# Kernel optimization log

Measured on AMD Instinct MI355X. Metric: run time of the kernel, lower is better.

Reference implementation:

```python
import jax, jax.numpy as jnp
from jax import lax
import numpy as np

N_INPUTS = 2048
UNITS = 2048
L = 8
FANIN = 4096
TOTAL = N_INPUTS + L * UNITS  # 18432, size of flattened outputs vector


def setup_inputs() -> dict:
    key = jax.random.key(0)
    k1, k2, k3, k4 = jax.random.split(key, 4)
    x = jax.random.normal(k1, (N_INPUTS,), dtype=jnp.float32)
    node_inds = jax.random.randint(k2, (L, FANIN), 0, TOTAL, dtype=jnp.int32)
    # 0.02 scale keeps tanh out of deep saturation (matches small evolved weights)
    Ws = jax.random.normal(k3, (L, FANIN, UNITS), dtype=jnp.float32) * 0.02
    bs = jax.random.normal(k4, (L, UNITS), dtype=jnp.float32) * 0.02
    return {"x": x, "node_inds": node_inds, "Ws": Ws, "bs": bs}


def reference(x, node_inds, Ws, bs):
    # Flattened shared state vector, zero-initialized like the tf.Variable.
    outputs = jnp.zeros((TOTAL,), dtype=x.dtype)
    start = 0  # static python offset: out_update_inds are contiguous ranges
    for i in range(L):
        # scatter_nd_update of x into contiguous slice == dynamic_update_slice
        outputs = lax.dynamic_update_slice(outputs, x, (start,))
        start += x.shape[0]
        # gather node-specific indices then tiny Dense + tanh
        gathered = jnp.take(outputs, node_inds[i])          # [FANIN]
        x = jnp.tanh(gathered @ Ws[i] + bs[i])              # [UNITS]
    return x
```

## Files before the change

kernel.cpp:

```cpp
#include <hip/hip_runtime.h>
#include <cmath>

#define N_INPUTS 2048
#define UNITS    2048
#define L_LAYERS 8
#define FANIN    4096
#define TOTAL    18432

#define NTHREADS 256
#define RK       16
#define KC       (FANIN / RK)
#define JTILE    1024
#define P_BLOCKS (2 * KC)

__device__ __forceinline__ float col_reduce(const float* __restrict__ P, int col)
{
    int lane = threadIdx.x & 63;
    float s = 0.f;
    #pragma unroll
    for (int m = 0; m < KC / 64; ++m)
        s += P[(size_t)(lane + m * 64) * UNITS + col];
    #pragma unroll
    for (int off = 32; off; off >>= 1)
        s += __shfl_down(s, off, 64);
    return __shfl(s, 0, 64);
}

__global__ __launch_bounds__(NTHREADS) void layer_kernel(
    int layer,
    const float* __restrict__ x,
    const int*   __restrict__ node_inds,
    const float* __restrict__ Ws,
    const float* __restrict__ bs,
    float*       __restrict__ outputs,
    const float* __restrict__ Pprev,
    float*       __restrict__ Pcur)
{
    const int b    = blockIdx.x;
    const int t    = threadIdx.x;
    const int wv   = t >> 6;
    const int lane = t & 63;
    const int jhalf = b & 1;
    const int kc    = b >> 1;

    __shared__ float gsh[RK];

    {
        int col = b * 4 + wv;
        if (layer == 0) {
            if (lane == 0) outputs[col] = x[col];
        } else {
            float s = col_reduce(Pprev, col);
            float y = tanhf(s + bs[(layer - 1) * UNITS + col]);
            if (lane == 0) outputs[(size_t)layer * UNITS + col] = y;
        }
    }

    #pragma unroll
    for (int j = 0; j < 4; ++j) {
        int q   = wv * 4 + j;
        int idx = node_inds[layer * FANIN + kc * RK + q];
        float g;
        if (layer == 0) {
            g = (idx < N_INPUTS) ? x[idx] : 0.f;
        } else if (idx < layer * UNITS) {
            g = outputs[idx];
        } else if (idx < (layer + 1) * UNITS) {
            int col = idx - layer * UNITS;
            float s = col_reduce(Pprev, col);
            g = tanhf(s + bs[(layer - 1) * UNITS + col]);
        } else {
            g = 0.f;
        }
        if (lane == 0) gsh[q] = g;
    }
    __syncthreads();

    const int jbase = jhalf * JTILE + t * 4;
    const float4* W4 = (const float4*)(
        Ws + ((size_t)layer * FANIN + (size_t)kc * RK) * UNITS + jbase);

    float4 a; a.x = 0.f; a.y = 0.f; a.z = 0.f; a.w = 0.f;
    #pragma unroll
    for (int k = 0; k < RK; ++k) {
        float  g = gsh[k];
        float4 w = W4[(size_t)k * (UNITS / 4)];
        a.x += g * w.x; a.y += g * w.y; a.z += g * w.z; a.w += g * w.w;
    }
    *(float4*)(Pcur + (size_t)kc * UNITS + jbase) = a;
}

__global__ __launch_bounds__(NTHREADS) void tail_kernel(
    const float* __restrict__ Pprev,
    const float* __restrict__ bs,
    float*       __restrict__ out)
{
    int wv   = threadIdx.x >> 6;
    int lane = threadIdx.x & 63;
    int col  = blockIdx.x * 4 + wv;
    float s = col_reduce(Pprev, col);
    float y = tanhf(s + bs[(L_LAYERS - 1) * UNITS + col]);
    if (lane == 0) out[col] = y;
}

extern "C" void kernel_launch(void* const* d_in, const int* in_sizes, int n_in,
                              void* d_out, int out_size, void* d_ws, size_t ws_size,
                              hipStream_t stream) {
    const float* x         = (const float*)d_in[0];
    const int*   node_inds = (const int*)  d_in[1];
    const float* Ws        = (const float*)d_in[2];
    const float* bs        = (const float*)d_in[3];
    float*       out       = (float*)d_out;
    float*       ws        = (float*)d_ws;

    float* outputs = ws;
    float* P0      = ws + TOTAL;
    float* P1      = P0 + (size_t)KC * UNITS;

    float* pbuf[2] = { P0, P1 };

    for (int i = 0; i < L_LAYERS; ++i) {
        layer_kernel<<<P_BLOCKS, NTHREADS, 0, stream>>>(
            i, x, node_inds, Ws, bs, outputs,
            pbuf[(i + 1) & 1],
            pbuf[i & 1]);
    }
    tail_kernel<<<UNITS / 4, NTHREADS, 0, stream>>>(
        pbuf[(L_LAYERS - 1) & 1], bs, out);
}
```

Baseline: 417.8 us.

## Fuse all layers into one cooperative persistent kernel with register weight prefetch

Replaces the per-layer kernel launches and the tail kernel with a single cooperative kernel that uses grid-wide syncs between layers. Each block keeps its weight tile in registers and prefetches the next layer's weights and indices before the grid sync, so weight loads can overlap the synchronization. This removes launch gaps, but adds grid-sync cost and register pressure, and keeps the original multi-launch path as a fallback if the cooperative launch fails.

```diff
diff --git a/kernel.cpp b/kernel.cpp
--- a/kernel.cpp
+++ b/kernel.cpp
@@ -1,5 +1,8 @@
 #include <hip/hip_runtime.h>
+#include <hip/hip_cooperative_groups.h>
 #include <cmath>
+
+namespace cg = cooperative_groups;
 
 #define N_INPUTS 2048
 #define UNITS    2048
@@ -24,6 +27,109 @@
     for (int off = 32; off; off >>= 1)
         s += __shfl_down(s, off, 64);
     return __shfl(s, 0, 64);
+}
+
+__global__ __launch_bounds__(NTHREADS, 2) void fused_kernel(
+    const float* __restrict__ x,
+    const int*   __restrict__ node_inds,
+    const float* __restrict__ Ws,
+    const float* __restrict__ bs,
+    float*       __restrict__ outputs,
+    float*       __restrict__ out,
+    float*       __restrict__ P0,
+    float*       __restrict__ P1)
+{
+    cg::grid_group grid = cg::this_grid();
+
+    const int b     = blockIdx.x;
+    const int t     = threadIdx.x;
+    const int wv    = t >> 6;
+    const int lane  = t & 63;
+    const int jhalf = b & 1;
+    const int kc    = b >> 1;
+    const int jbase = jhalf * JTILE + t * 4;
+
+    __shared__ float gsh[RK];
+
+    float* pb[2] = { P0, P1 };
+
+    float4 w[RK];
+    {
+        const float4* W4 = (const float4*)(
+            Ws + ((size_t)kc * RK) * UNITS + jbase);
+        #pragma unroll
+        for (int k = 0; k < RK; ++k)
+            w[k] = W4[(size_t)k * (UNITS / 4)];
+    }
+    int4 nidx = *(const int4*)(node_inds + kc * RK + wv * 4);
+
+    for (int lay = 0; lay < L_LAYERS; ++lay) {
+        const float* Pprev = pb[(lay + 1) & 1];
+        float*       Pcur  = pb[lay & 1];
+
+        if (lay > 0) grid.sync();
+
+        {
+            int col = b * 4 + wv;
+            if (lay == 0) {
+                if (lane == 0) outputs[col] = x[col];
+            } else {
+                float s = col_reduce(Pprev, col);
+                float y = tanhf(s + bs[(lay - 1) * UNITS + col]);
+                if (lane == 0) outputs[(size_t)lay * UNITS + col] = y;
+            }
+        }
+
+        {
+            int idxs[4] = { nidx.x, nidx.y, nidx.z, nidx.w };
+            #pragma unroll
+            for (int j = 0; j < 4; ++j) {
+                int q   = wv * 4 + j;
+                int idx = idxs[j];
+                float g;
+                if (lay == 0) {
+                    g = (idx < N_INPUTS) ? x[idx] : 0.f;
+                } else if (idx < lay * UNITS) {
+                    g = outputs[idx];
+                } else if (idx < (lay + 1) * UNITS) {
+                    int col = idx - lay * UNITS;
+                    float s = col_reduce(Pprev, col);
+                    g = tanhf(s + bs[(lay - 1) * UNITS + col]);
+                } else {
+                    g = 0.f;
+                }
+                if (lane == 0) gsh[q] = g;
+            }
+        }
+        __syncthreads();
+
+        float4 a; a.x = 0.f; a.y = 0.f; a.z = 0.f; a.w = 0.f;
+        #pragma unroll
+        for (int k = 0; k < RK; ++k) {
+            float g = gsh[k];
+            a.x += g * w[k].x; a.y += g * w[k].y;
+            a.z += g * w[k].z; a.w += g * w[k].w;
+        }
+        *(float4*)(Pcur + (size_t)kc * UNITS + jbase) = a;
+
+        if (lay + 1 < L_LAYERS) {
+            const float4* W4n = (const float4*)(
+                Ws + ((size_t)(lay + 1) * FANIN + (size_t)kc * RK) * UNITS + jbase);
+            #pragma unroll
+            for (int k = 0; k < RK; ++k)
+                w[k] = W4n[(size_t)k * (UNITS / 4)];
+            nidx = *(const int4*)(
+                node_inds + (lay + 1) * FANIN + kc * RK + wv * 4);
+        }
+    }
+
+    grid.sync();
+    {
+        int col = b * 4 + wv;
+        float s = col_reduce(pb[(L_LAYERS - 1) & 1], col);
+        float y = tanhf(s + bs[(L_LAYERS - 1) * UNITS + col]);
+        if (lane == 0) out[col] = y;
+    }
 }
 
 __global__ __launch_bounds__(NTHREADS) void layer_kernel(
@@ -84,8 +190,8 @@
     #pragma unroll
     for (int k = 0; k < RK; ++k) {
         float  g = gsh[k];
-        float4 w = W4[(size_t)k * (UNITS / 4)];
-        a.x += g * w.x; a.y += g * w.y; a.z += g * w.z; a.w += g * w.w;
+        float4 wv4 = W4[(size_t)k * (UNITS / 4)];
+        a.x += g * wv4.x; a.y += g * wv4.y; a.z += g * wv4.z; a.w += g * wv4.w;
     }
     *(float4*)(Pcur + (size_t)kc * UNITS + jbase) = a;
 }
@@ -117,14 +223,21 @@
     float* P0      = ws + TOTAL;
     float* P1      = P0 + (size_t)KC * UNITS;
 
-    float* pbuf[2] = { P0, P1 };
-
-    for (int i = 0; i < L_LAYERS; ++i) {
-        layer_kernel<<<P_BLOCKS, NTHREADS, 0, stream>>>(
-            i, x, node_inds, Ws, bs, outputs,
-            pbuf[(i + 1) & 1],
-            pbuf[i & 1]);
-    }
-    tail_kernel<<<UNITS / 4, NTHREADS, 0, stream>>>(
-        pbuf[(L_LAYERS - 1) & 1], bs, out);
-}
+    void* args[8] = { (void*)&x, (void*)&node_inds, (void*)&Ws, (void*)&bs,
+                      (void*)&outputs, (void*)&out, (void*)&P0, (void*)&P1 };
+
+    hipError_t e = hipLaunchCooperativeKernel(
+        (const void*)fused_kernel, dim3(P_BLOCKS), dim3(NTHREADS),
+        args, 0, stream);
+
+    if (e != hipSuccess) {
+        float* pbuf[2] = { P0, P1 };
+        for (int i = 0; i < L_LAYERS; ++i) {
+            layer_kernel<<<P_BLOCKS, NTHREADS, 0, stream>>>(
+                i, x, node_inds, Ws, bs, outputs,
+                pbuf[(i + 1) & 1], pbuf[i & 1]);
+        }
+        tail_kernel<<<UNITS / 4, NTHREADS, 0, stream>>>(
+            pbuf[(L_LAYERS - 1) & 1], bs, out);
+    }
+}
```

After: 868.3 us. 108% more time.

## Prefetch weights before gather, transpose partial-sum layout, split columns four ways

Applied to the files above, without the earlier changes.

Each block now issues all of its weight loads into registers before the gather and column-reduce work, so the HBM stream overlaps that latency-bound phase. The partial-sum buffer is transposed to column-major [UNITS][KC], which makes col_reduce reads contiguous per wave but makes the partial-sum stores strided. Blocks split the output columns into four parts, doubling the block count, and launch bounds request higher occupancy. Risks are the scattered 4-byte stores and more register pressure from holding the weights.

```diff
diff --git a/kernel.cpp b/kernel.cpp
--- a/kernel.cpp
+++ b/kernel.cpp
@@ -10,8 +10,9 @@
 #define NTHREADS 256
 #define RK       16
 #define KC       (FANIN / RK)
-#define JTILE    1024
-#define P_BLOCKS (2 * KC)
+#define JPARTS   4
+#define JTILE    (UNITS / JPARTS)
+#define P_BLOCKS (KC * JPARTS)
 
 __device__ __forceinline__ float col_reduce(const float* __restrict__ P, int col)
 {
@@ -19,14 +20,14 @@
     float s = 0.f;
     #pragma unroll
     for (int m = 0; m < KC / 64; ++m)
-        s += P[(size_t)(lane + m * 64) * UNITS + col];
+        s += P[(size_t)col * KC + lane + m * 64];
     #pragma unroll
     for (int off = 32; off; off >>= 1)
         s += __shfl_down(s, off, 64);
     return __shfl(s, 0, 64);
 }
 
-__global__ __launch_bounds__(NTHREADS) void layer_kernel(
+__global__ __launch_bounds__(NTHREADS, 4) void layer_kernel(
     int layer,
     const float* __restrict__ x,
     const int*   __restrict__ node_inds,
@@ -40,13 +41,23 @@
     const int t    = threadIdx.x;
     const int wv   = t >> 6;
     const int lane = t & 63;
-    const int jhalf = b & 1;
-    const int kc    = b >> 1;
+    const int kc   = b >> 2;
+    const int jp   = b & 3;
+    const int jbase = jp * JTILE + t * 2;
 
     __shared__ float gsh[RK];
 
-    {
-        int col = b * 4 + wv;
+    float2 w[RK];
+    const float2* W2 = (const float2*)(
+        Ws + ((size_t)layer * FANIN + (size_t)kc * RK) * UNITS + jbase);
+    #pragma unroll
+    for (int k = 0; k < RK; ++k)
+        w[k] = W2[(size_t)k * (UNITS / 2)];
+
+    int4 nidx = *(const int4*)(node_inds + layer * FANIN + kc * RK + wv * 4);
+
+    if (wv < 2) {
+        int col = b * 2 + wv;
         if (layer == 0) {
             if (lane == 0) outputs[col] = x[col];
         } else {
@@ -56,38 +67,38 @@
         }
     }
 
-    #pragma unroll
-    for (int j = 0; j < 4; ++j) {
-        int q   = wv * 4 + j;
-        int idx = node_inds[layer * FANIN + kc * RK + q];
-        float g;
-        if (layer == 0) {
-            g = (idx < N_INPUTS) ? x[idx] : 0.f;
-        } else if (idx < layer * UNITS) {
-            g = outputs[idx];
-        } else if (idx < (layer + 1) * UNITS) {
-            int col = idx - layer * UNITS;
-            float s = col_reduce(Pprev, col);
-            g = tanhf(s + bs[(layer - 1) * UNITS + col]);
-        } else {
-            g = 0.f;
+    {
+        int idxs[4] = { nidx.x, nidx.y, nidx.z, nidx.w };
+        #pragma unroll
+        for (int j = 0; j < 4; ++j) {
+            int q   = wv * 4 + j;
+            int idx = idxs[j];
+            float g;
+            if (layer == 0) {
+                g = (idx < N_INPUTS) ? x[idx] : 0.f;
+            } else if (idx < layer * UNITS) {
+                g = outputs[idx];
+            } else if (idx < (layer + 1) * UNITS) {
+                int col = idx - layer * UNITS;
+                float s = col_reduce(Pprev, col);
+                g = tanhf(s + bs[(layer - 1) * UNITS + col]);
+            } else {
+                g = 0.f;
+            }
+            if (lane == 0) gsh[q] = g;
         }
-        if (lane == 0) gsh[q] = g;
     }
     __syncthreads();
 
-    const int jbase = jhalf * JTILE + t * 4;
-    const float4* W4 = (const float4*)(
-        Ws + ((size_t)layer * FANIN + (size_t)kc * RK) * UNITS + jbase);
-
-    float4 a; a.x = 0.f; a.y = 0.f; a.z = 0.f; a.w = 0.f;
+    float ax = 0.f, ay = 0.f;
     #pragma unroll
     for (int k = 0; k < RK; ++k) {
-        float  g = gsh[k];
-        float4 w = W4[(size_t)k * (UNITS / 4)];
-        a.x += g * w.x; a.y += g * w.y; a.z += g * w.z; a.w += g * w.w;
+        float g = gsh[k];
+        ax += g * w[k].x;
+        ay += g * w[k].y;
     }
-    *(float4*)(Pcur + (size_t)kc * UNITS + jbase) = a;
+    Pcur[(size_t)jbase       * KC + kc] = ax;
+    Pcur[(size_t)(jbase + 1) * KC + kc] = ay;
 }
 
 __global__ __launch_bounds__(NTHREADS) void tail_kernel(
```

Result: faster. 399.6 us (-4.3%).

## Replace partial-sum matrix and column reductions with atomic accumulation

Applied to the files above, without the earlier changes.

Each block now reduces its 64-row K-chunk in shared memory and atomically adds into a 2048-wide accumulator. This replaces writing a 256x2048 partial matrix and re-reducing columns for every gathered index. Three rotating accumulator buffers let each layer zero the next buffer while reading the previous one, so gathers become single loads plus tanh. Weight loads are issued into registers before the gather and the sync, to hide latency. The cost is float atomic contention and run-to-run rounding differences from unordered accumulation.

```diff
diff --git a/kernel.cpp b/kernel.cpp
--- a/kernel.cpp
+++ b/kernel.cpp
@@ -8,99 +8,106 @@
 #define TOTAL    18432
 
 #define NTHREADS 256
-#define RK       16
+#define RK       64
 #define KC       (FANIN / RK)
-#define JTILE    1024
-#define P_BLOCKS (2 * KC)
+#define JTILE    128
+#define JPARTS   (UNITS / JTILE)
+#define P_BLOCKS (KC * JPARTS)
 
-__device__ __forceinline__ float col_reduce(const float* __restrict__ P, int col)
-{
-    int lane = threadIdx.x & 63;
-    float s = 0.f;
-    #pragma unroll
-    for (int m = 0; m < KC / 64; ++m)
-        s += P[(size_t)(lane + m * 64) * UNITS + col];
-    #pragma unroll
-    for (int off = 32; off; off >>= 1)
-        s += __shfl_down(s, off, 64);
-    return __shfl(s, 0, 64);
-}
-
-__global__ __launch_bounds__(NTHREADS) void layer_kernel(
+__global__ __launch_bounds__(NTHREADS, 4) void layer_kernel(
     int layer,
     const float* __restrict__ x,
     const int*   __restrict__ node_inds,
     const float* __restrict__ Ws,
     const float* __restrict__ bs,
     float*       __restrict__ outputs,
-    const float* __restrict__ Pprev,
-    float*       __restrict__ Pcur)
+    const float* __restrict__ accPrev,
+    float*       __restrict__ accCur,
+    float*       __restrict__ accNext)
 {
-    const int b    = blockIdx.x;
-    const int t    = threadIdx.x;
-    const int wv   = t >> 6;
-    const int lane = t & 63;
-    const int jhalf = b & 1;
-    const int kc    = b >> 1;
+    const int b  = blockIdx.x;
+    const int t  = threadIdx.x;
+    const int kc = b >> 4;
+    const int jp = b & 15;
+    const int jbase = jp * JTILE;
+    const int g  = t >> 5;
+    const int c0 = (t & 31) * 4;
 
-    __shared__ float gsh[RK];
+    __shared__ float  gsh[RK];
+    __shared__ float4 red[8][32];
 
-    {
-        int col = b * 4 + wv;
+    int idx = 0;
+    if (t < RK) idx = node_inds[layer * FANIN + kc * RK + t];
+
+    const float* Wp = Ws
+        + ((size_t)layer * FANIN + (size_t)kc * RK + (size_t)g * 8) * UNITS
+        + jbase + c0;
+    float4 w[8];
+    #pragma unroll
+    for (int r = 0; r < 8; ++r)
+        w[r] = *(const float4*)(Wp + (size_t)r * UNITS);
+
+    if (t < RK) {
+        float v;
         if (layer == 0) {
-            if (lane == 0) outputs[col] = x[col];
+            v = (idx < N_INPUTS) ? x[idx] : 0.f;
+        } else if (idx < layer * UNITS) {
+            v = outputs[idx];
+        } else if (idx < (layer + 1) * UNITS) {
+            int col = idx - layer * UNITS;
+            v = tanhf(accPrev[col] + bs[(layer - 1) * UNITS + col]);
         } else {
-            float s = col_reduce(Pprev, col);
-            float y = tanhf(s + bs[(layer - 1) * UNITS + col]);
-            if (lane == 0) outputs[(size_t)layer * UNITS + col] = y;
+            v = 0.f;
+        }
+        gsh[t] = v;
+    }
+
+    if (kc == 0 && t < JTILE) {
+        int col = jbase + t;
+        if (layer == 0) {
+            outputs[col] = x[col];
+        } else {
+            float y = tanhf(accPrev[col] + bs[(layer - 1) * UNITS + col]);
+            outputs[(size_t)layer * UNITS + col] = y;
         }
     }
 
-    #pragma unroll
-    for (int j = 0; j < 4; ++j) {
-        int q   = wv * 4 + j;
-        int idx = node_inds[layer * FANIN + kc * RK + q];
-        float g;
-        if (layer == 0) {
-            g = (idx < N_INPUTS) ? x[idx] : 0.f;
-        } else if (idx < layer * UNITS) {
-            g = outputs[idx];
-        } else if (idx < (layer + 1) * UNITS) {
-            int col = idx - layer * UNITS;
-            float s = col_reduce(Pprev, col);
-            g = tanhf(s + bs[(layer - 1) * UNITS + col]);
-        } else {
-            g = 0.f;
-        }
-        if (lane == 0) gsh[q] = g;
-    }
+    if (t < 2) accNext[b * 2 + t] = 0.f;
+
     __syncthreads();
-
-    const int jbase = jhalf * JTILE + t * 4;
-    const float4* W4 = (const float4*)(
-        Ws + ((size_t)layer * FANIN + (size_t)kc * RK) * UNITS + jbase);
 
     float4 a; a.x = 0.f; a.y = 0.f; a.z = 0.f; a.w = 0.f;
     #pragma unroll
-    for (int k = 0; k < RK; ++k) {
-        float  g = gsh[k];
-        float4 w = W4[(size_t)k * (UNITS / 4)];
-        a.x += g * w.x; a.y += g * w.y; a.z += g * w.z; a.w += g * w.w;
+    for (int r = 0; r < 8; ++r) {
+        float gg = gsh[g * 8 + r];
+        a.x += gg * w[r].x; a.y += gg * w[r].y;
+        a.z += gg * w[r].z; a.w += gg * w[r].w;
     }
-    *(float4*)(Pcur + (size_t)kc * UNITS + jbase) = a;
+    red[g][t & 31] = a;
+    __syncthreads();
+
+    if (t < 32) {
+        float4 s = red[0][t];
+        #pragma unroll
+        for (int q = 1; q < 8; ++q) {
+            float4 r4 = red[q][t];
+            s.x += r4.x; s.y += r4.y; s.z += r4.z; s.w += r4.w;
+        }
+        int col = jbase + t * 4;
+        atomicAdd(accCur + col + 0, s.x);
+        atomicAdd(accCur + col + 1, s.y);
+        atomicAdd(accCur + col + 2, s.z);
+        atomicAdd(accCur + col + 3, s.w);
+    }
 }
 
 __global__ __launch_bounds__(NTHREADS) void tail_kernel(
-    const float* __restrict__ Pprev,
+    const float* __restrict__ acc,
     const float* __restrict__ bs,
     float*       __restrict__ out)
 {
-    int wv   = threadIdx.x >> 6;
-    int lane = threadIdx.x & 63;
-    int col  = blockIdx.x * 4 + wv;
-    float s = col_reduce(Pprev, col);
-    float y = tanhf(s + bs[(L_LAYERS - 1) * UNITS + col]);
-    if (lane == 0) out[col] = y;
+    int i = blockIdx.x * NTHREADS + threadIdx.x;
+    out[i] = tanhf(acc[i] + bs[(L_LAYERS - 1) * UNITS + i]);
 }
 
 extern "C" void kernel_launch(void* const* d_in, const int* in_sizes, int n_in,
@@ -114,17 +121,20 @@
     float*       ws        = (float*)d_ws;
 
     float* outputs = ws;
-    float* P0      = ws + TOTAL;
-    float* P1      = P0 + (size_t)KC * UNITS;
+    float* A0      = ws + TOTAL;
+    float* A1      = A0 + UNITS;
+    float* A2      = A1 + UNITS;
+    float* bufs[3] = { A0, A1, A2 };
 
-    float* pbuf[2] = { P0, P1 };
+    hipMemsetAsync(A0, 0, UNITS * sizeof(float), stream);
 
     for (int i = 0; i < L_LAYERS; ++i) {
         layer_kernel<<<P_BLOCKS, NTHREADS, 0, stream>>>(
             i, x, node_inds, Ws, bs, outputs,
-            pbuf[(i + 1) & 1],
-            pbuf[i & 1]);
+            bufs[(i + 2) % 3],
+            bufs[i % 3],
+            bufs[(i + 1) % 3]);
     }
-    tail_kernel<<<UNITS / 4, NTHREADS, 0, stream>>>(
-        pbuf[(L_LAYERS - 1) & 1], bs, out);
+    tail_kernel<<<UNITS / NTHREADS, NTHREADS, 0, stream>>>(
+        bufs[(L_LAYERS - 1) % 3], bs, out);
 }
```

Result: slower. 429.2 us (+2.7%).
